# Kernel tuning notes

Hardware: AMD Instinct MI355X
Metric: run time of the kernel (lower is better)

Reference implementation:

```python
import jax, jax.numpy as jnp
import numpy as np

TH, TW = 64, 64        # template_size (image shape)
OH, OW = 256, 256      # out_size
K = 3                  # spline order
PAD = 4                # hardcoded padding in module
OFF = PAD - (K + 1) // 2          # = 2
CX_OFF = (OH - TH) // 2           # centering_offset[0] = 96
CY_OFF = (OW - TW) // 2           # centering_offset[1] = 96
BATCH = 1024


def bspline3(p):
    # fast cubic B-spline basis, p: (B,) -> (B, 4)
    return jnp.stack([
        p ** 3 / 6,
        -p ** 3 / 2 + p ** 2 / 2 + p / 2 + 1.0 / 6,
        p ** 3 / 2 - p ** 2 + 2.0 / 3,
        (1 - p) ** 3 / 6,
    ], axis=-1)


def setup_inputs() -> dict:
    key = jax.random.key(0)
    k1, k2, k3 = jax.random.split(key, 3)
    coeffs = jax.random.normal(k1, (TH + 2 * PAD, TW + 2 * PAD), jnp.float32)
    x = (jax.random.normal(k2, (BATCH, 1, 1, 1), jnp.float32) - 0.5) * 10
    y = (jax.random.normal(k3, (BATCH, 1, 1, 1), jnp.float32) - 0.5) * 10
    return {"coeffs": coeffs, "x": x, "y": y}


def reference(coeffs, x, y):
    B = x.shape[0]
    # integer pixel shift (floor) and subpixel remainder
    px = jnp.floor(x[:, 0, 0, 0]).astype(jnp.int32)  # (B,)
    py = jnp.floor(y[:, 0, 0, 0]).astype(jnp.int32)  # (B,)
    sx = jnp.remainder(x[:, 0, 0, 0], 1.0)           # (B,)
    sy = jnp.remainder(y[:, 0, 0, 0], 1.0)           # (B,)

    bx = bspline3(sx)  # (B,4) basis along rows (i index)
    by = bspline3(sy)  # (B,4) basis along cols (j index)

    # (4,4,TH+1,TW+1) shifted coefficient windows
    slices = jnp.stack([
        jnp.stack([coeffs[i + OFF:i + OFF + TH + 1, j + OFF:j + OFF + TW + 1]
                   for j in range(K + 1)])
        for i in range(K + 1)])
    # blended template: (B, TH+1, TW+1)
    template = jnp.einsum('bi,bj,ijrc->brc', bx, by, slices)

    bi = jnp.arange(B)[:, None, None]

    # scatter along columns (dim 3 in torch): x_a[b, r, idx_a] = template[b, r, c]
    col = jnp.arange(TW + 1)
    idx_a = jnp.clip(col[None, None, :] + py[:, None, None] + CY_OFF + 1, 0, OW + 1)  # (B,1,TW+1)
    ri = jnp.arange(TH + 1)[None, :, None]
    x_a = jnp.zeros((B, OH + 2, OW + 2), template.dtype)
    x_a = x_a.at[bi, ri, idx_a].set(template)

    # scatter along rows (dim 2 in torch): x_b[b, idx_b, c] = x_a[b, r, c]
    row = jnp.arange(OH + 2)
    idx_b = jnp.clip(row[None, :, None] + px[:, None, None] + CX_OFF + 1, 0, OH + 1)  # (B,OH+2,1)
    ci = jnp.arange(OW + 2)[None, None, :]
    x_b = jnp.zeros_like(x_a).at[bi, idx_b, ci].set(x_a)

    return x_b[:, 1:-1, 1:-1][:, None]  # (B,1,OH,OW)
```

## Files before the change

kernel.cpp:

```cpp
#include <hip/hip_runtime.h>


#define CW 72
#define PATCH 65
#define PATCH_ELEMS (PATCH * PATCH)

__global__ __launch_bounds__(256) void spline2d_patch(
    const float* __restrict__ coeffs,
    const float* __restrict__ x,
    const float* __restrict__ y,
    float* __restrict__ out)
{
    const int b = blockIdx.x;

    const float xv = x[b];
    const float yv = y[b];
    const float fx = floorf(xv), fy = floorf(yv);
    const int   px = (int)fx,    py = (int)fy;
    const float sx = xv - fx,    sy = yv - fy;

    float wx[4], wy[4];
    {
        const float p = sx, p2 = p * p, p3 = p2 * p, q = 1.0f - p;
        wx[0] = p3 * (1.0f / 6.0f);
        wx[1] = -0.5f * p3 + 0.5f * p2 + 0.5f * p + (1.0f / 6.0f);
        wx[2] = 0.5f * p3 - p2 + (2.0f / 3.0f);
        wx[3] = q * q * q * (1.0f / 6.0f);
    }
    {
        const float p = sy, p2 = p * p, p3 = p2 * p, q = 1.0f - p;
        wy[0] = p3 * (1.0f / 6.0f);
        wy[1] = -0.5f * p3 + 0.5f * p2 + 0.5f * p + (1.0f / 6.0f);
        wy[2] = 0.5f * p3 - p2 + (2.0f / 3.0f);
        wy[3] = q * q * q * (1.0f / 6.0f);
    }

    const int R0 = px + 96;
    const int C0 = py + 96;
    float* __restrict__ ob = out + (size_t)b * 65536;

    for (int e = threadIdx.x; e < PATCH_ELEMS; e += 256) {
        const int r = e / PATCH;
        const int c = e - r * PATCH;
        const int R = R0 + r;
        const int C = C0 + c;
        if ((unsigned)R < 256u && (unsigned)C < 256u) {
            const float* p0 = coeffs + (r + 2) * CW + (c + 2);
            float v = 0.0f;
#pragma unroll
            for (int i = 0; i < 4; ++i) {
                const float* row = p0 + i * CW;
                const float s = row[0] * wy[0] + row[1] * wy[1] +
                                row[2] * wy[2] + row[3] * wy[3];
                v = fmaf(wx[i], s, v);
            }
            ob[R * 256 + C] = v;
        }
    }
}

extern "C" void kernel_launch(void* const* d_in, const int* in_sizes, int n_in,
                              void* d_out, int out_size, void* d_ws, size_t ws_size,
                              hipStream_t stream) {
    const float* coeffs = (const float*)d_in[0];
    const float* x      = (const float*)d_in[1];
    const float* y      = (const float*)d_in[2];
    float* out = (float*)d_out;

    hipMemsetAsync(out, 0, (size_t)out_size * sizeof(float), stream);

    const int batch = in_sizes[1];
    spline2d_patch<<<batch, 256, 0, stream>>>(coeffs, x, y, out);
}
```

Before: 268.3 us.

## Fuse zero-fill into spline kernel with per-row-segment blocks and float4 stores

Drops the separate full-output memset and has each block own a 16-row band of one batch image, writing every output element exactly once with float4 stores (zeros outside the 65x65 patch, spline values inside). Bands that do not touch the patch take an early-exit path that only writes zeros. This removes the double write of the patch region and the extra launch, at the cost of 16x more blocks and some divergent per-element bounds checks in the patch columns.

```diff
diff --git a/kernel.cpp b/kernel.cpp
--- a/kernel.cpp
+++ b/kernel.cpp
@@ -2,23 +2,43 @@
 
 
 #define CW 72
-#define PATCH 65
-#define PATCH_ELEMS (PATCH * PATCH)
 
-__global__ __launch_bounds__(256) void spline2d_patch(
+__global__ __launch_bounds__(256) void spline2d_fused(
     const float* __restrict__ coeffs,
     const float* __restrict__ x,
     const float* __restrict__ y,
     float* __restrict__ out)
 {
-    const int b = blockIdx.x;
+    const int blk    = blockIdx.x;
+    const int b      = blk >> 4;
+    const int seg    = blk & 15;
+    const int Rstart = seg << 4;
 
     const float xv = x[b];
     const float yv = y[b];
     const float fx = floorf(xv), fy = floorf(yv);
     const int   px = (int)fx,    py = (int)fy;
-    const float sx = xv - fx,    sy = yv - fy;
+    const int   R0 = px + 96;
+    const int   C0 = py + 96;
 
+    const int t         = threadIdx.x;
+    const int rowInPass = t >> 6;
+    const int col4      = (t & 63) << 2;
+
+    float* __restrict__ obase =
+        out + ((size_t)b << 16) + ((size_t)Rstart << 8);
+
+    const float4 z4 = make_float4(0.f, 0.f, 0.f, 0.f);
+
+    if (R0 > Rstart + 15 || R0 + 64 < Rstart) {
+#pragma unroll
+        for (int u = 0; u < 4; ++u) {
+            *reinterpret_cast<float4*>(obase + (u << 10) + (rowInPass << 8) + col4) = z4;
+        }
+        return;
+    }
+
+    const float sx = xv - fx, sy = yv - fy;
     float wx[4], wy[4];
     {
         const float p = sx, p2 = p * p, p3 = p2 * p, q = 1.0f - p;
@@ -35,27 +55,33 @@
         wy[3] = q * q * q * (1.0f / 6.0f);
     }
 
-    const int R0 = px + 96;
-    const int C0 = py + 96;
-    float* __restrict__ ob = out + (size_t)b * 65536;
-
-    for (int e = threadIdx.x; e < PATCH_ELEMS; e += 256) {
-        const int r = e / PATCH;
-        const int c = e - r * PATCH;
-        const int R = R0 + r;
-        const int C = C0 + c;
-        if ((unsigned)R < 256u && (unsigned)C < 256u) {
-            const float* p0 = coeffs + (r + 2) * CW + (c + 2);
-            float v = 0.0f;
 #pragma unroll
-            for (int i = 0; i < 4; ++i) {
-                const float* row = p0 + i * CW;
-                const float s = row[0] * wy[0] + row[1] * wy[1] +
-                                row[2] * wy[2] + row[3] * wy[3];
-                v = fmaf(wx[i], s, v);
+    for (int u = 0; u < 4; ++u) {
+        const int R = Rstart + (u << 2) + rowInPass;
+        const int r = R - R0;
+        float4 v = z4;
+        if ((unsigned)r <= 64u) {
+            const int cb = col4 - C0;
+            float vv[4];
+#pragma unroll
+            for (int e = 0; e < 4; ++e) {
+                const int c = cb + e;
+                float s = 0.0f;
+                if ((unsigned)c <= 64u) {
+                    const float* p0 = coeffs + (r + 2) * CW + (c + 2);
+#pragma unroll
+                    for (int i = 0; i < 4; ++i) {
+                        const float* row = p0 + i * CW;
+                        const float rs = row[0] * wy[0] + row[1] * wy[1] +
+                                         row[2] * wy[2] + row[3] * wy[3];
+                        s = fmaf(wx[i], rs, s);
+                    }
+                }
+                vv[e] = s;
             }
-            ob[R * 256 + C] = v;
+            v = make_float4(vv[0], vv[1], vv[2], vv[3]);
         }
+        *reinterpret_cast<float4*>(obase + (u << 10) + (rowInPass << 8) + col4) = v;
     }
 }
 
@@ -67,8 +93,6 @@
     const float* y      = (const float*)d_in[2];
     float* out = (float*)d_out;
 
-    hipMemsetAsync(out, 0, (size_t)out_size * sizeof(float), stream);
-
     const int batch = in_sizes[1];
-    spline2d_patch<<<batch, 256, 0, stream>>>(coeffs, x, y, out);
+    spline2d_fused<<<batch * 16, 256, 0, stream>>>(coeffs, x, y, out);
 }
```

After: 334.4 us. 24.6% more time.
